# Optimization experiments

Hardware: AMD Instinct MI355X
Metric: run time of the kernel (lower is better)

The kernel has to match this reference:

```python
import jax, jax.numpy as jnp
import numpy as np

L, N, H_IN, H = 512, 32, 1024, 1024


def _mk_params(key, in_dim, hid):
    ks = jax.random.split(key, 7)
    s_in = 1.0 / np.sqrt(in_dim)
    s_h = 1.0 / np.sqrt(hid)
    return dict(
        Wmx=jax.random.uniform(ks[0], (hid, in_dim), jnp.float32, -s_in, s_in),
        Wmh=jax.random.uniform(ks[1], (hid, hid), jnp.float32, -s_h, s_h),
        bmx=jax.random.uniform(ks[2], (hid,), jnp.float32, -s_in, s_in),
        bmh=jax.random.uniform(ks[3], (hid,), jnp.float32, -s_h, s_h),
        Wgx=jax.random.uniform(ks[4], (4 * hid, in_dim), jnp.float32, -s_in, s_in),
        Wgm=jax.random.uniform(ks[5], (4 * hid, hid), jnp.float32, -s_h, s_h),
        bg=jax.random.uniform(ks[6], (4 * hid,), jnp.float32, -s_h, s_h),
    )


def setup_inputs() -> dict:
    key = jax.random.key(0)
    k_in, k0, k1 = jax.random.split(key, 3)
    inp = {"inputs": jax.random.normal(k_in, (L, N, H_IN), jnp.float32)}
    for i, (k, d) in enumerate([(k0, H_IN), (k1, H)]):
        p = _mk_params(k, d, H)
        for name, v in p.items():
            inp[f"{name}{i}"] = v
    return inp


def _run_layer(xs, state, Wmx, Wmh, bmx, bmh, Wgx, Wgm, bg):
    # xs: (L, N, in_dim); state: ((N,H),(N,H))
    def step(carry, x_t):
        h, c = carry
        m = (x_t @ Wmx.T + bmx) * (h @ Wmh.T + bmh)  # multiplicative intermediate
        g = x_t @ Wgx.T + m @ Wgm.T + bg             # (N, 4H)
        i_g, f_g, z_g, o_g = jnp.split(g, 4, axis=-1)
        c_new = jax.nn.sigmoid(f_g) * c + jax.nn.sigmoid(i_g) * jnp.tanh(z_g)
        h_new = jax.nn.sigmoid(o_g) * jnp.tanh(c_new)
        return (h_new, c_new), h_new

    (h, c), ys = jax.lax.scan(step, state, xs)
    return ys, (h, c)


def reference(inputs, Wmx0, Wmh0, bmx0, bmh0, Wgx0, Wgm0, bg0,
              Wmx1, Wmh1, bmx1, bmh1, Wgx1, Wgm1, bg1):
    zeros = jnp.zeros((N, H), inputs.dtype)
    state = (zeros, zeros)
    # NOTE: original torch code carries hidden_state across layers (quirk kept).
    ys, state = _run_layer(inputs, state, Wmx0, Wmh0, bmx0, bmh0, Wgx0, Wgm0, bg0)
    hs, cs = [state[0]], [state[1]]
    ys, state = _run_layer(ys, state, Wmx1, Wmh1, bmx1, bmh1, Wgx1, Wgm1, bg1)
    hs.append(state[0]); cs.append(state[1])
    return ys, (jnp.stack(hs), jnp.stack(cs))
```

## Files before the change

### kernel.cpp

```cpp
#include <hip/hip_runtime.h>
#include <hip/hip_bf16.h>


typedef unsigned short u16;
typedef unsigned int u32;
typedef unsigned long long u64;
typedef __attribute__((ext_vector_type(8))) short bf16x8;
typedef __attribute__((ext_vector_type(4))) float f32x4;
typedef __attribute__((ext_vector_type(4))) unsigned int u32x4;

#define LSEQ 512
#define NB   32
#define HD   1024
#define G4   4096
#define YSZ  (LSEQ*NB*HD)
#define NH32 (NB*HD)
#define SEG  64
#define NSEG (LSEQ/SEG)
#define PERSIST_LDS 163840

#define ATOMIC_RLX __ATOMIC_RELAXED
#define SCOPE_AGT __HIP_MEMORY_SCOPE_AGENT

__device__ __forceinline__ float b2f(u16 u) {
    u32 i = ((u32)u) << 16; float f; __builtin_memcpy(&f, &i, 4); return f;
}
__device__ __forceinline__ u16 f2b(float f) {
    u32 x; __builtin_memcpy(&x, &f, 4);
    return (u16)((x + 0x7fffu + ((x >> 16) & 1u)) >> 16);
}
__device__ __forceinline__ int SW(int row, int byte) { return byte ^ ((row & 7) << 4); }

__device__ __forceinline__ void pollwait(const u32* flags, u32 target) {
    const int lane = threadIdx.x & 63;
    const u64* p = (const u64*)flags + (size_t)lane * 16;
    for (;;) {
        u64 v = __hip_atomic_load(p, ATOMIC_RLX, SCOPE_AGT);
        u32 lo = (u32)v, hi = (u32)(v >> 32);
        if (__all(lo >= target && hi >= target)) break;
        __builtin_amdgcn_s_sleep(4);
    }
    asm volatile("" ::: "memory");
}

__device__ __forceinline__ void load_row16(const char* base, u32x4* dst) {
#pragma unroll
    for (int kt = 0; kt < 32; ++kt) {
        u64 a = (u64)(base + kt * 64);
        asm volatile("global_load_dwordx4 %0, %1, off sc0 sc1"
                     : "=v"(dst[kt]) : "v"(a));
    }
    asm volatile("s_waitcnt vmcnt(0)" ::: "memory");
    __builtin_amdgcn_sched_barrier(0);
}

__device__ __forceinline__ void store_transposed(u16* ebuf, int rowbase, int colbase,
                                                 const u16 mu[4]) {
    const int lane = threadIdx.x & 63;
    u32 wlo = (u32)mu[0] | ((u32)mu[1] << 16);
    u32 whi = (u32)mu[2] | ((u32)mu[3] << 16);
    const int rl = lane >> 2;
    const int r = rl & 3, lks = rl >> 2;
    u64 outv = 0;
#pragma unroll
    for (int i = 0; i < 4; ++i) {
        int s = lks * 16 + (lane & 3) * 4 + i;
        u32 a  = (u32)__shfl((int)wlo, s);
        u32 bb = (u32)__shfl((int)whi, s);
        u32 pick = (r & 2) ? bb : a;
        u32 val = (r & 1) ? (pick >> 16) : (pick & 0xFFFFu);
        outv |= (u64)val << (16 * i);
    }
    u64* dst = (u64*)(ebuf + (size_t)(rowbase + rl) * HD + colbase + (lane & 3) * 4);
    __hip_atomic_store(dst, outv, ATOMIC_RLX, SCOPE_AGT);
}

__global__ void k_cvt(const float* __restrict__ s, u16* __restrict__ d, long n) {
    long i = (long)blockIdx.x * blockDim.x + threadIdx.x;
    long stride = (long)gridDim.x * blockDim.x;
    for (; i < n; i += stride) d[i] = f2b(s[i]);
}

template<typename XT> __device__ __forceinline__ bf16x8 ld8(const XT* p);
template<> __device__ __forceinline__ bf16x8 ld8<u16>(const u16* p) {
    return *(const bf16x8*)p;
}
template<> __device__ __forceinline__ bf16x8 ld8<float>(const float* p) {
    float4 a = *(const float4*)p, b = *(const float4*)(p + 4);
    bf16x8 r;
    r[0]=(short)f2b(a.x); r[1]=(short)f2b(a.y); r[2]=(short)f2b(a.z); r[3]=(short)f2b(a.w);
    r[4]=(short)f2b(b.x); r[5]=(short)f2b(b.y); r[6]=(short)f2b(b.z); r[7]=(short)f2b(b.w);
    return r;
}

template<typename XT>
__global__ __launch_bounds__(256) void k_gemm(
    const XT* __restrict__ X, const u16* __restrict__ W,
    const float* __restrict__ bias, u16* __restrict__ Out, int ldo)
{
    __shared__ u16 As[128][40];
    __shared__ u16 Bs[128][40];
    int bm = blockIdx.y, bn = blockIdx.x;
    int tid = threadIdx.x;
    int w = tid >> 6, lane = tid & 63;
    int wm = w >> 1, wn = w & 1;
    int l16 = lane & 15, lk = lane >> 4;

    f32x4 acc[4][4];
    #pragma unroll
    for (int i = 0; i < 4; ++i)
        #pragma unroll
        for (int j = 0; j < 4; ++j) acc[i][j] = (f32x4){0.f, 0.f, 0.f, 0.f};

    for (int kt = 0; kt < 32; ++kt) {
        __syncthreads();
        #pragma unroll
        for (int c = 0; c < 2; ++c) {
            int cid = tid + c * 256;
            int rrow = cid >> 2, kc = (cid & 3) * 8;
            *(bf16x8*)(&As[rrow][kc]) = ld8<XT>(X + (long)(bm * 128 + rrow) * HD + kt * 32 + kc);
            *(bf16x8*)(&Bs[rrow][kc]) = ld8<u16>(W + (long)(bn * 128 + rrow) * HD + kt * 32 + kc);
        }
        __syncthreads();
        bf16x8 af[4], bfr[4];
        #pragma unroll
        for (int mt = 0; mt < 4; ++mt)
            af[mt] = *(const bf16x8*)(&As[wm * 64 + mt * 16 + l16][lk * 8]);
        #pragma unroll
        for (int nt = 0; nt < 4; ++nt)
            bfr[nt] = *(const bf16x8*)(&Bs[wn * 64 + nt * 16 + l16][lk * 8]);
        #pragma unroll
        for (int mt = 0; mt < 4; ++mt)
            #pragma unroll
            for (int nt = 0; nt < 4; ++nt)
                acc[mt][nt] = __builtin_amdgcn_mfma_f32_16x16x32_bf16(
                    af[mt], bfr[nt], acc[mt][nt], 0, 0, 0);
    }
    #pragma unroll
    for (int mt = 0; mt < 4; ++mt)
        #pragma unroll
        for (int nt = 0; nt < 4; ++nt) {
            int colg = bn * 128 + wn * 64 + nt * 16 + l16;
            float bv = bias[colg];
            #pragma unroll
            for (int r = 0; r < 4; ++r) {
                int rowg = bm * 128 + wm * 64 + mt * 16 + lk * 4 + r;
                Out[(long)rowg * ldo + colg] = f2b(acc[mt][nt][r] + bv);
            }
        }
}

__global__ __launch_bounds__(256, 1) void k_persist(
    const u16* __restrict__ Wmhb, const float* __restrict__ bmh,
    const u16* __restrict__ Wgmb,
    const u16* __restrict__ Ab,
    const u16* __restrict__ Gxb,
    u16* eh, u16* em,
    float* __restrict__ cbuf,
    u16* __restrict__ yb, float* __restrict__ yf,
    float* __restrict__ tail,
    int l, int tbc, int tbi, u32* fM, u32* fH)
{
    extern __shared__ __align__(16) char lds[];
    const int tid = threadIdx.x;
    const int b = blockIdx.x;
    const int w = tid >> 6, lane = tid & 63;
    const int l16 = lane & 15, lk = lane >> 4;

    for (int it = 0; it < 32; ++it) {
        int cch = tid + it * 256;
        int lr = cch >> 7, k8 = cch & 127;
        int g = lr >> 4, c16 = lr & 15;
        bf16x8 v = *(const bf16x8*)(Wgmb + (long)(g * 1024 + 16 * b + c16) * HD + k8 * 8);
        *(bf16x8*)(lds + SW(lr, lr * 2048 + k8 * 16)) = v;
    }
    for (int it = 0; it < 8; ++it) {
        int cch = tid + it * 256;
        int lr = cch >> 7, k8 = cch & 127;
        bf16x8 v = *(const bf16x8*)(Wmhb + (long)(16 * b + lr) * HD + k8 * 8);
        *(bf16x8*)(lds + 131072 + SW(lr, lr * 2048 + k8 * 16)) = v;
    }
    __syncthreads();

    const int colg = 16 * b + l16;
    const int rt = w & 1;
    const bool isP1 = (w >= 2);

    const float bcol = bmh[colg];
    const char* hbase = (const char*)eh + (size_t)(rt * 16 + l16) * 2048 + lk * 16;
    const char* mbase = (const char*)em + (size_t)(rt * 16 + l16) * 2048 + lk * 16;
    f32x4 creg = (f32x4){0.f, 0.f, 0.f, 0.f};
    if (!isP1)
        #pragma unroll
        for (int r = 0; r < 4; ++r)
            creg[r] = cbuf[(rt * 16 + lk * 4 + r) * HD + colg];

    for (int t = 0; t < SEG; ++t) {
        const u32 gt = (u32)(tbc + t);
        u16 atv[4];
        u16 gxv[4][4];
        if (isP1) {
            const u16* At = Ab + (long)(tbi + t) * NH32;
            #pragma unroll
            for (int r = 0; r < 4; ++r)
                atv[r] = At[(rt * 16 + lk * 4 + r) * HD + colg];
        } else {
            const u16* Gx = Gxb + (long)t * NB * G4;
            #pragma unroll
            for (int g = 0; g < 4; ++g)
                #pragma unroll
                for (int r = 0; r < 4; ++r)
                    gxv[g][r] = Gx[(long)(rt * 16 + lk * 4 + r) * G4 + g * 1024 + colg];
        }
        if (w == 2) pollwait(fH, gt);
        __syncthreads();
        if (isP1) {
            u32x4 hv[32];
            load_row16(hbase, hv);
            f32x4 acc = (f32x4){0.f, 0.f, 0.f, 0.f};
            #pragma unroll
            for (int kt = 0; kt < 32; ++kt) {
                union { u32x4 q; bf16x8 v; } u;
                u.q = hv[kt];
                bf16x8 bfrag = *(const bf16x8*)(lds + 131072 +
                                SW(l16, l16 * 2048 + kt * 64 + lk * 16));
                acc = __builtin_amdgcn_mfma_f32_16x16x32_bf16(u.v, bfrag, acc, 0, 0, 0);
            }
            u16 mu[4];
            #pragma unroll
            for (int r = 0; r < 4; ++r)
                mu[r] = f2b(b2f(atv[r]) * (acc[r] + bcol));
            store_transposed(em, rt * 16, 16 * b, mu);
            asm volatile("s_waitcnt vmcnt(0)" ::: "memory");
            if (lane == 0)
                __hip_atomic_store(fM + b * 32 + rt, gt + 1, ATOMIC_RLX, SCOPE_AGT);
        }
        if (w == 0) pollwait(fM, gt + 1);
        __syncthreads();
        if (!isP1) {
            u32x4 mv[32];
            load_row16(mbase, mv);
            f32x4 gacc[4];
            #pragma unroll
            for (int g = 0; g < 4; ++g) gacc[g] = (f32x4){0.f, 0.f, 0.f, 0.f};
            #pragma unroll
            for (int kt = 0; kt < 32; ++kt) {
                union { u32x4 q; bf16x8 v; } u;
                u.q = mv[kt];
                #pragma unroll
                for (int g = 0; g < 4; ++g) {
                    int lr = g * 16 + l16;
                    bf16x8 bfrag = *(const bf16x8*)(lds + SW(lr, lr * 2048 + kt * 64 + lk * 16));
                    gacc[g] = __builtin_amdgcn_mfma_f32_16x16x32_bf16(u.v, bfrag, gacc[g], 0, 0, 0);
                }
            }
            float hn[4];
            u16 hu[4];
            #pragma unroll
            for (int r = 0; r < 4; ++r) {
                float ig = gacc[0][r] + b2f(gxv[0][r]);
                float fg = gacc[1][r] + b2f(gxv[1][r]);
                float zg = gacc[2][r] + b2f(gxv[2][r]);
                float og = gacc[3][r] + b2f(gxv[3][r]);
                float si = 1.f / (1.f + expf(-ig));
                float sf = 1.f / (1.f + expf(-fg));
                float so = 1.f / (1.f + expf(-og));
                float cn = sf * creg[r] + si * tanhf(zg);
                hn[r] = so * tanhf(cn);
                creg[r] = cn;
                hu[r] = f2b(hn[r]);
            }
            store_transposed(eh, rt * 16, 16 * b, hu);
            asm volatile("s_waitcnt vmcnt(0)" ::: "memory");
            if (lane == 0)
                __hip_atomic_store(fH + b * 32 + rt, gt + 1, ATOMIC_RLX, SCOPE_AGT);
            #pragma unroll
            for (int r = 0; r < 4; ++r) {
                int row = rt * 16 + lk * 4 + r;
                long yidx = (long)(tbi + t) * NH32 + (long)row * HD + colg;
                if (yb) yb[yidx] = f2b(hn[r]); else yf[yidx] = hn[r];
                if (tbi + t == LSEQ - 1) {
                    tail[(long)l * NH32 + row * HD + colg] = hn[r];
                    tail[2L * NH32 + (long)l * NH32 + row * HD + colg] = creg[r];
                }
            }
        }
    }
    if (!isP1)
        #pragma unroll
        for (int r = 0; r < 4; ++r)
            cbuf[(rt * 16 + lk * 4 + r) * HD + colg] = creg[r];
}

extern "C" void kernel_launch(void* const* d_in, const int* in_sizes, int n_in,
                              void* d_out, int out_size, void* d_ws, size_t ws_size,
                              hipStream_t stream) {
    (void)in_sizes; (void)n_in; (void)out_size; (void)ws_size;
    const float* inputs = (const float*)d_in[0];
    const float* Wmx[2] = {(const float*)d_in[1], (const float*)d_in[8]};
    const float* Wmh[2] = {(const float*)d_in[2], (const float*)d_in[9]};
    const float* bmx[2] = {(const float*)d_in[3], (const float*)d_in[10]};
    const float* bmh[2] = {(const float*)d_in[4], (const float*)d_in[11]};
    const float* Wgx[2] = {(const float*)d_in[5], (const float*)d_in[12]};
    const float* Wgm[2] = {(const float*)d_in[6], (const float*)d_in[13]};
    const float* bg[2]  = {(const float*)d_in[7], (const float*)d_in[14]};
    float* out = (float*)d_out;

    char* ws = (char*)d_ws;
    const long MB = 1024L * 1024L;
    u16* Wmxb[2] = {(u16*)(ws + 0 * MB),  (u16*)(ws + 2 * MB)};
    u16* Wmhb[2] = {(u16*)(ws + 4 * MB),  (u16*)(ws + 6 * MB)};
    u16* Wgxb[2] = {(u16*)(ws + 8 * MB),  (u16*)(ws + 16 * MB)};
    u16* Wgmb[2] = {(u16*)(ws + 24 * MB), (u16*)(ws + 32 * MB)};
    u16* Yb  = (u16*)(ws + 40 * MB);
    u16* Ab  = (u16*)(ws + 72 * MB);
    u16* Gxb = (u16*)(ws + 104 * MB);
    char* ex = ws + 120 * MB;
    u16* exch_h = (u16*)ex;
    u16* exch_m = (u16*)(ex + 65536);
    float* cbuf = (float*)(ex + 131072);
    u32* fM     = (u32*)(ex + 262144);
    u32* fH     = (u32*)(ex + 262144 + 8192);

    hipFuncSetAttribute((const void*)k_persist,
                        hipFuncAttributeMaxDynamicSharedMemorySize, PERSIST_LDS);

    hipMemsetAsync(ex, 0, 262144 + 16384, stream);

    k_cvt<<<512, 256, 0, stream>>>(Wmx[0], Wmxb[0], (long)HD * HD);
    k_cvt<<<512, 256, 0, stream>>>(Wmx[1], Wmxb[1], (long)HD * HD);
    k_cvt<<<512, 256, 0, stream>>>(Wmh[0], Wmhb[0], (long)HD * HD);
    k_cvt<<<512, 256, 0, stream>>>(Wmh[1], Wmhb[1], (long)HD * HD);
    k_cvt<<<1024, 256, 0, stream>>>(Wgx[0], Wgxb[0], (long)G4 * HD);
    k_cvt<<<1024, 256, 0, stream>>>(Wgx[1], Wgxb[1], (long)G4 * HD);
    k_cvt<<<1024, 256, 0, stream>>>(Wgm[0], Wgmb[0], (long)G4 * HD);
    k_cvt<<<1024, 256, 0, stream>>>(Wgm[1], Wgmb[1], (long)G4 * HD);

    for (int l = 0; l < 2; ++l) {
        if (l == 0)
            k_gemm<float><<<dim3(8, 128), 256, 0, stream>>>(inputs, Wmxb[0], bmx[0], Ab, HD);
        else
            k_gemm<u16><<<dim3(8, 128), 256, 0, stream>>>(Yb, Wmxb[1], bmx[1], Ab, HD);
        for (int s = 0; s < NSEG; ++s) {
            if (l == 0)
                k_gemm<float><<<dim3(32, 16), 256, 0, stream>>>(
                    inputs + (long)s * SEG * NB * HD, Wgxb[0], bg[0], Gxb, G4);
            else
                k_gemm<u16><<<dim3(32, 16), 256, 0, stream>>>(
                    Yb + (long)s * SEG * NB * HD, Wgxb[1], bg[1], Gxb, G4);
            k_persist<<<64, 256, PERSIST_LDS, stream>>>(
                Wmhb[l], bmh[l], Wgmb[l], Ab, Gxb,
                exch_h, exch_m, cbuf,
                l ? nullptr : Yb, l ? out : nullptr, out + YSZ,
                l, l * LSEQ + s * SEG, s * SEG, fM, fH);
        }
    }
}
```

Measured before the change: 13.88 ms.

## Decouple P1/P2 waves with per-wave flag polling, wider transposed stores

Splits the persistent recurrent kernel's per-step loop into separate loops for the h@Wmh waves and the gate waves. Each wave polls its own dependency flags directly instead of having one wave poll followed by block-wide __syncthreads. The transposed exchange store now writes 16-byte dwordx4 from half the lanes instead of 8-byte atomics from all lanes. The poll sleep interval is also shortened. This is meant to cut barrier and store latency on the serial critical path, at the cost of more polling traffic and relying on per-wave memory ordering.

Measured after the change: 14.80 ms. 6.6% more time.

```diff
diff --git a/kernel.cpp b/kernel.cpp
--- a/kernel.cpp
+++ b/kernel.cpp
@@ -38,7 +38,7 @@
         u64 v = __hip_atomic_load(p, ATOMIC_RLX, SCOPE_AGT);
         u32 lo = (u32)v, hi = (u32)(v >> 32);
         if (__all(lo >= target && hi >= target)) break;
-        __builtin_amdgcn_s_sleep(4);
+        __builtin_amdgcn_s_sleep(1);
     }
     asm volatile("" ::: "memory");
 }
@@ -54,25 +54,38 @@
     __builtin_amdgcn_sched_barrier(0);
 }
 
-__device__ __forceinline__ void store_transposed(u16* ebuf, int rowbase, int colbase,
-                                                 const u16 mu[4]) {
-    const int lane = threadIdx.x & 63;
+__device__ __forceinline__ void store_t16(u16* ebuf, int rowbase, int colbase,
+                                          const u16 mu[4]) {
+    const int d = threadIdx.x & 63;
     u32 wlo = (u32)mu[0] | ((u32)mu[1] << 16);
     u32 whi = (u32)mu[2] | ((u32)mu[3] << 16);
-    const int rl = lane >> 2;
-    const int r = rl & 3, lks = rl >> 2;
-    u64 outv = 0;
+    const int Rl = d >> 1, half = d & 1;
+    const int lks = Rl >> 2, r = Rl & 3;
+    u32x4 outv;
 #pragma unroll
-    for (int i = 0; i < 4; ++i) {
-        int s = lks * 16 + (lane & 3) * 4 + i;
-        u32 a  = (u32)__shfl((int)wlo, s);
-        u32 bb = (u32)__shfl((int)whi, s);
-        u32 pick = (r & 2) ? bb : a;
-        u32 val = (r & 1) ? (pick >> 16) : (pick & 0xFFFFu);
-        outv |= (u64)val << (16 * i);
-    }
-    u64* dst = (u64*)(ebuf + (size_t)(rowbase + rl) * HD + colbase + (lane & 3) * 4);
-    __hip_atomic_store(dst, outv, ATOMIC_RLX, SCOPE_AGT);
+    for (int p = 0; p < 4; ++p) {
+        u32 v0, v1;
+        {
+            int s = lks * 16 + half * 8 + 2 * p;
+            u32 a = (u32)__shfl((int)wlo, s);
+            u32 bb = (u32)__shfl((int)whi, s);
+            u32 pick = (r & 2) ? bb : a;
+            v0 = (r & 1) ? (pick >> 16) : (pick & 0xFFFFu);
+        }
+        {
+            int s = lks * 16 + half * 8 + 2 * p + 1;
+            u32 a = (u32)__shfl((int)wlo, s);
+            u32 bb = (u32)__shfl((int)whi, s);
+            u32 pick = (r & 2) ? bb : a;
+            v1 = (r & 1) ? (pick >> 16) : (pick & 0xFFFFu);
+        }
+        outv[p] = v0 | (v1 << 16);
+    }
+    if (d < 32) {
+        u64 addr = (u64)ebuf + (size_t)(rowbase + Rl) * 2048 + colbase * 2 + half * 16;
+        asm volatile("global_store_dwordx4 %0, %1, off sc0 sc1"
+                     :: "v"(addr), "v"(outv) : "memory");
+    }
 }
 
 __global__ void k_cvt(const float* __restrict__ s, u16* __restrict__ d, long n) {
@@ -195,26 +208,15 @@
         for (int r = 0; r < 4; ++r)
             creg[r] = cbuf[(rt * 16 + lk * 4 + r) * HD + colg];
 
-    for (int t = 0; t < SEG; ++t) {
-        const u32 gt = (u32)(tbc + t);
-        u16 atv[4];
-        u16 gxv[4][4];
-        if (isP1) {
+    if (isP1) {
+        for (int t = 0; t < SEG; ++t) {
+            const u32 gt = (u32)(tbc + t);
             const u16* At = Ab + (long)(tbi + t) * NH32;
+            u16 atv[4];
             #pragma unroll
             for (int r = 0; r < 4; ++r)
                 atv[r] = At[(rt * 16 + lk * 4 + r) * HD + colg];
-        } else {
-            const u16* Gx = Gxb + (long)t * NB * G4;
-            #pragma unroll
-            for (int g = 0; g < 4; ++g)
-                #pragma unroll
-                for (int r = 0; r < 4; ++r)
-                    gxv[g][r] = Gx[(long)(rt * 16 + lk * 4 + r) * G4 + g * 1024 + colg];
-        }
-        if (w == 2) pollwait(fH, gt);
-        __syncthreads();
-        if (isP1) {
+            pollwait(fH, gt);
             u32x4 hv[32];
             load_row16(hbase, hv);
             f32x4 acc = (f32x4){0.f, 0.f, 0.f, 0.f};
@@ -230,14 +232,22 @@
             #pragma unroll
             for (int r = 0; r < 4; ++r)
                 mu[r] = f2b(b2f(atv[r]) * (acc[r] + bcol));
-            store_transposed(em, rt * 16, 16 * b, mu);
+            store_t16(em, rt * 16, 16 * b, mu);
             asm volatile("s_waitcnt vmcnt(0)" ::: "memory");
             if (lane == 0)
                 __hip_atomic_store(fM + b * 32 + rt, gt + 1, ATOMIC_RLX, SCOPE_AGT);
         }
-        if (w == 0) pollwait(fM, gt + 1);
-        __syncthreads();
-        if (!isP1) {
+    } else {
+        for (int t = 0; t < SEG; ++t) {
+            const u32 gt = (u32)(tbc + t);
+            const u16* Gx = Gxb + (long)t * NB * G4;
+            u16 gxv[4][4];
+            #pragma unroll
+            for (int g = 0; g < 4; ++g)
+                #pragma unroll
+                for (int r = 0; r < 4; ++r)
+                    gxv[g][r] = Gx[(long)(rt * 16 + lk * 4 + r) * G4 + g * 1024 + colg];
+            pollwait(fM, gt + 1);
             u32x4 mv[32];
             load_row16(mbase, mv);
             f32x4 gacc[4];
@@ -270,7 +280,7 @@
                 creg[r] = cn;
                 hu[r] = f2b(hn[r]);
             }
-            store_transposed(eh, rt * 16, 16 * b, hu);
+            store_t16(eh, rt * 16, 16 * b, hu);
             asm volatile("s_waitcnt vmcnt(0)" ::: "memory");
             if (lane == 0)
                 __hip_atomic_store(fH + b * 32 + rt, gt + 1, ATOMIC_RLX, SCOPE_AGT);
@@ -285,11 +295,10 @@
                 }
             }
         }
-    }
-    if (!isP1)
         #pragma unroll
         for (int r = 0; r < 4; ++r)
             cbuf[(rt * 16 + lk * 4 + r) * HD + colg] = creg[r];
+    }
 }
 
 extern "C" void kernel_launch(void* const* d_in, const int* in_sizes, int n_in,
```

## Overlap next-segment input GEMMs with persistent recurrence in a hybrid kernel

Applied to the files above, without the earlier changes.

Merges the per-segment input-projection GEMMs (Gx and A) into the persistent recurrence launch. Blocks 0-63 run the recurrence for the current segment while extra blocks compute the next segment's projections into double-buffered Gx/A buffers. This removes the serial GEMM launches between segments and the per-layer full-sequence A GEMM. The cost is that GEMM blocks now share the GPU with the latency-sensitive persistent blocks. The persistent blocks busy-wait on flags, so this depends on all 64 of them staying resident alongside the GEMM blocks, and the GEMM blocks may steal bandwidth from them.

Result: no change. 14.13 ms (+1.8%).

```diff
diff --git a/kernel.cpp b/kernel.cpp
--- a/kernel.cpp
+++ b/kernel.cpp
@@ -18,6 +18,8 @@
 #define SEG  64
 #define NSEG (LSEQ/SEG)
 #define PERSIST_LDS 163840
+#define GXBLK 512
+#define ABLK  128
 
 #define ATOMIC_RLX __ATOMIC_RELAXED
 #define SCOPE_AGT __HIP_MEMORY_SCOPE_AGENT
@@ -94,13 +96,12 @@
 }
 
 template<typename XT>
-__global__ __launch_bounds__(256) void k_gemm(
-    const XT* __restrict__ X, const u16* __restrict__ W,
-    const float* __restrict__ bias, u16* __restrict__ Out, int ldo)
-{
-    __shared__ u16 As[128][40];
-    __shared__ u16 Bs[128][40];
-    int bm = blockIdx.y, bn = blockIdx.x;
+__device__ void gemm_tile(char* ldsbuf,
+                          const XT* __restrict__ X, const u16* __restrict__ W,
+                          const float* __restrict__ bias, u16* __restrict__ Out,
+                          int ldo, int bm, int bn) {
+    u16 (*As)[40] = (u16(*)[40])ldsbuf;
+    u16 (*Bs)[40] = (u16(*)[40])(ldsbuf + 10240);
     int tid = threadIdx.x;
     int w = tid >> 6, lane = tid & 63;
     int wm = w >> 1, wn = w & 1;
@@ -150,20 +151,46 @@
         }
 }
 
-__global__ __launch_bounds__(256, 1) void k_persist(
+template<typename XT>
+__global__ __launch_bounds__(256) void k_gemm(
+    const XT* __restrict__ X, const u16* __restrict__ W,
+    const float* __restrict__ bias, u16* __restrict__ Out, int ldo)
+{
+    __shared__ char ldsbuf[20480];
+    gemm_tile<XT>(ldsbuf, X, W, bias, Out, ldo, blockIdx.y, blockIdx.x);
+}
+
+template<typename XT>
+__global__ __launch_bounds__(256, 1) void k_hybrid(
     const u16* __restrict__ Wmhb, const float* __restrict__ bmh,
     const u16* __restrict__ Wgmb,
     const u16* __restrict__ Ab,
     const u16* __restrict__ Gxb,
-    u16* eh, u16* em,
-    float* __restrict__ cbuf,
+    u16* eh, u16* em, float* __restrict__ cbuf,
     u16* __restrict__ yb, float* __restrict__ yf,
     float* __restrict__ tail,
-    int l, int tbc, int tbi, u32* fM, u32* fH)
+    int l, int tbc, int tbi, u32* fM, u32* fH,
+    const XT* __restrict__ Xs1, const u16* __restrict__ Wgxb,
+    const float* __restrict__ bg, u16* __restrict__ Gx1,
+    const u16* __restrict__ Wmxb, const float* __restrict__ bmx,
+    u16* __restrict__ A1)
 {
     extern __shared__ __align__(16) char lds[];
+    const int bid = blockIdx.x;
+
+    if (bid >= 64) {
+        int idx = bid - 64;
+        if (idx < GXBLK) {
+            gemm_tile<XT>(lds, Xs1, Wgxb, bg, Gx1, G4, idx >> 5, idx & 31);
+        } else {
+            idx -= GXBLK;
+            gemm_tile<XT>(lds, Xs1, Wmxb, bmx, A1, HD, idx >> 3, idx & 7);
+        }
+        return;
+    }
+
     const int tid = threadIdx.x;
-    const int b = blockIdx.x;
+    const int b = bid;
     const int w = tid >> 6, lane = tid & 63;
     const int l16 = lane & 15, lk = lane >> 4;
 
@@ -200,7 +227,7 @@
         u16 atv[4];
         u16 gxv[4][4];
         if (isP1) {
-            const u16* At = Ab + (long)(tbi + t) * NH32;
+            const u16* At = Ab + (long)t * NH32;
             #pragma unroll
             for (int r = 0; r < 4; ++r)
                 atv[r] = At[(rt * 16 + lk * 4 + r) * HD + colg];
@@ -312,17 +339,19 @@
     u16* Wmhb[2] = {(u16*)(ws + 4 * MB),  (u16*)(ws + 6 * MB)};
     u16* Wgxb[2] = {(u16*)(ws + 8 * MB),  (u16*)(ws + 16 * MB)};
     u16* Wgmb[2] = {(u16*)(ws + 24 * MB), (u16*)(ws + 32 * MB)};
-    u16* Yb  = (u16*)(ws + 40 * MB);
-    u16* Ab  = (u16*)(ws + 72 * MB);
-    u16* Gxb = (u16*)(ws + 104 * MB);
-    char* ex = ws + 120 * MB;
+    u16* Yb    = (u16*)(ws + 40 * MB);
+    u16* Gxb[2] = {(u16*)(ws + 72 * MB), (u16*)(ws + 88 * MB)};
+    u16* Abf[2] = {(u16*)(ws + 104 * MB), (u16*)(ws + 108 * MB)};
+    char* ex = ws + 112 * MB;
     u16* exch_h = (u16*)ex;
     u16* exch_m = (u16*)(ex + 65536);
     float* cbuf = (float*)(ex + 131072);
     u32* fM     = (u32*)(ex + 262144);
     u32* fH     = (u32*)(ex + 262144 + 8192);
 
-    hipFuncSetAttribute((const void*)k_persist,
+    hipFuncSetAttribute((const void*)&k_hybrid<float>,
+                        hipFuncAttributeMaxDynamicSharedMemorySize, PERSIST_LDS);
+    hipFuncSetAttribute((const void*)&k_hybrid<u16>,
                         hipFuncAttributeMaxDynamicSharedMemorySize, PERSIST_LDS);
 
     hipMemsetAsync(ex, 0, 262144 + 16384, stream);
@@ -337,22 +366,36 @@
     k_cvt<<<1024, 256, 0, stream>>>(Wgm[1], Wgmb[1], (long)G4 * HD);
 
     for (int l = 0; l < 2; ++l) {
-        if (l == 0)
-            k_gemm<float><<<dim3(8, 128), 256, 0, stream>>>(inputs, Wmxb[0], bmx[0], Ab, HD);
-        else
-            k_gemm<u16><<<dim3(8, 128), 256, 0, stream>>>(Yb, Wmxb[1], bmx[1], Ab, HD);
+        if (l == 0) {
+            k_gemm<float><<<dim3(32, 16), 256, 0, stream>>>(inputs, Wgxb[0], bg[0], Gxb[0], G4);
+            k_gemm<float><<<dim3(8, 16), 256, 0, stream>>>(inputs, Wmxb[0], bmx[0], Abf[0], HD);
+        } else {
+            k_gemm<u16><<<dim3(32, 16), 256, 0, stream>>>(Yb, Wgxb[1], bg[1], Gxb[0], G4);
+            k_gemm<u16><<<dim3(8, 16), 256, 0, stream>>>(Yb, Wmxb[1], bmx[1], Abf[0], HD);
+        }
         for (int s = 0; s < NSEG; ++s) {
-            if (l == 0)
-                k_gemm<float><<<dim3(32, 16), 256, 0, stream>>>(
-                    inputs + (long)s * SEG * NB * HD, Wgxb[0], bg[0], Gxb, G4);
-            else
-                k_gemm<u16><<<dim3(32, 16), 256, 0, stream>>>(
-                    Yb + (long)s * SEG * NB * HD, Wgxb[1], bg[1], Gxb, G4);
-            k_persist<<<64, 256, PERSIST_LDS, stream>>>(
-                Wmhb[l], bmh[l], Wgmb[l], Ab, Gxb,
-                exch_h, exch_m, cbuf,
-                l ? nullptr : Yb, l ? out : nullptr, out + YSZ,
-                l, l * LSEQ + s * SEG, s * SEG, fM, fH);
-        }
-    }
-}
+            bool pf = (s + 1 < NSEG);
+            int grid = pf ? (64 + GXBLK + ABLK) : 64;
+            int cur = s & 1, nxt = (s + 1) & 1;
+            u16* ybp = l ? nullptr : Yb;
+            float* yfp = l ? out : nullptr;
+            if (l == 0) {
+                const float* xs1 = inputs + (long)(s + 1) * SEG * NB * HD;
+                k_hybrid<float><<<grid, 256, PERSIST_LDS, stream>>>(
+                    Wmhb[0], bmh[0], Wgmb[0], Abf[cur], Gxb[cur],
+                    exch_h, exch_m, cbuf, ybp, yfp, out + YSZ,
+                    0, s * SEG, s * SEG, fM, fH,
+                    pf ? xs1 : inputs, Wgxb[0], bg[0], Gxb[nxt],
+                    Wmxb[0], bmx[0], Abf[nxt]);
+            } else {
+                const u16* xs1 = Yb + (long)(s + 1) * SEG * NB * HD;
+                k_hybrid<u16><<<grid, 256, PERSIST_LDS, stream>>>(
+                    Wmhb[1], bmh[1], Wgmb[1], Abf[cur], Gxb[cur],
+                    exch_h, exch_m, cbuf, ybp, yfp, out + YSZ,
+                    1, LSEQ + s * SEG, s * SEG, fM, fH,
+                    pf ? xs1 : Yb, Wgxb[1], bg[1], Gxb[nxt],
+                    Wmxb[1], bmx[1], Abf[nxt]);
+            }
+        }
+    }
+}
```
